# Kernel optimization log

Measured on AMD Instinct MI355X. Metric: run time of the kernel, lower is better.

Reference implementation:

```python
import jax, jax.numpy as jnp
import numpy as np

B, S, D, H, F = 4, 2048, 512, 8, 2048
HD = D // H
SCALE = HD ** -0.5


def layernorm(x, g, b, eps=1e-5):
    mu = jnp.mean(x, axis=-1, keepdims=True)
    var = jnp.var(x, axis=-1, keepdims=True)
    return (x - mu) * jax.lax.rsqrt(var + eps) * g + b


def setup_inputs() -> dict:
    key = jax.random.key(0)
    ks = jax.random.split(key, 10)
    s = 0.02
    return {
        "x": jax.random.normal(ks[0], (B, S, D), jnp.float32),
        "w_qkv": jax.random.normal(ks[1], (D, 3 * D), jnp.float32) * s,
        "b_qkv": jnp.zeros((3 * D,), jnp.float32),
        "w_o": jax.random.normal(ks[2], (D, D), jnp.float32) * s,
        "b_o": jnp.zeros((D,), jnp.float32),
        "w1": jax.random.normal(ks[3], (D, F), jnp.float32) * s,
        "b1": jnp.zeros((F,), jnp.float32),
        "w2": jax.random.normal(ks[4], (F, D), jnp.float32) * s,
        "b2": jnp.zeros((D,), jnp.float32),
        "g1": jnp.ones((D,), jnp.float32),
        "be1": jnp.zeros((D,), jnp.float32),
        "g2": jnp.ones((D,), jnp.float32),
        "be2": jnp.zeros((D,), jnp.float32),
    }


def reference(x, w_qkv, b_qkv, w_o, b_o, w1, b1, w2, b2, g1, be1, g2, be2):
    res = x
    qkv = x @ w_qkv + b_qkv                       # [B,S,3D]
    q, k, v = jnp.split(qkv, 3, axis=-1)          # each [B,S,D]
    # head partition: [B,S,D] -> [B,H,S,hd]
    def split_heads(t):
        return t.reshape(B, S, H, HD).transpose(0, 2, 1, 3)
    q, k, v = map(split_heads, (q, k, v))
    scores = jnp.einsum('bhqc,bhkc->bhqk', q, k) * SCALE
    weights = jax.nn.softmax(scores, axis=-1)
    out = jnp.einsum('bhqk,bhkc->bhqc', weights, v)
    out = out.transpose(0, 2, 1, 3).reshape(B, S, D)  # merge heads
    out = out @ w_o + b_o
    out = layernorm(out + res, g1, be1)
    res = out
    out = jax.nn.gelu(out @ w1 + b1, approximate=False) @ w2 + b2
    out = layernorm(out + res, g2, be2)
    return out
```

## Files before the change

kernel.cpp:

```cpp
#include <hip/hip_runtime.h>
#include <math.h>

constexpr int B = 4, S = 2048, D = 512, H = 8, HD = 64, F = 2048;
constexpr int M = B * S;
constexpr float C_QK = 0.125f * 1.44269504088896340736f;

typedef __bf16 bf16x8 __attribute__((ext_vector_type(8)));
typedef float  f32x4  __attribute__((ext_vector_type(4)));
typedef float  f32x16 __attribute__((ext_vector_type(16)));

static __device__ __forceinline__ short f2bf(float f) {
  return __builtin_bit_cast(short, (__bf16)f);
}

static __device__ __forceinline__ void gload16(const void* g, void* l) {
  __builtin_amdgcn_global_load_lds(
      (const __attribute__((address_space(1))) unsigned int*)g,
      (__attribute__((address_space(3))) unsigned int*)l, 16, 0, 0);
}

__global__ __launch_bounds__(256)
void prep_all(const float* __restrict__ x, short* __restrict__ xb,
              const float* __restrict__ w_qkv, short* __restrict__ wtq,
              const float* __restrict__ w_o,  short* __restrict__ wto,
              const float* __restrict__ w1,   short* __restrict__ wt1,
              const float* __restrict__ w2,   short* __restrict__ wt2) {
  __shared__ float tl[32][33];
  const int id = blockIdx.x;
  const int t = threadIdx.x;
  if (id < 4096) {
    int i = id * 256 + t;
    float4 v = ((const float4*)x)[i];
    ((short4*)xb)[i] = make_short4(f2bf(v.x), f2bf(v.y), f2bf(v.z), f2bf(v.w));
    return;
  }
  const float* in; short* out; int R, C, bx, by;
  if (id < 4864)      { int k = id - 4096; in = w_qkv; out = wtq; R = 512;  C = 1536; bx = k % 48; by = k / 48; }
  else if (id < 5120) { int k = id - 4864; in = w_o;   out = wto; R = 512;  C = 512;  bx = k % 16; by = k / 16; }
  else if (id < 6144) { int k = id - 5120; in = w1;    out = wt1; R = 512;  C = 2048; bx = k % 64; by = k / 64; }
  else                { int k = id - 6144; in = w2;    out = wt2; R = 2048; C = 512;  bx = k % 16; by = k / 16; }
  const int r0 = by * 32, c0 = bx * 32;
  const int tr = t >> 3, tc4 = (t & 7) * 4;
  float4 v = *(const float4*)&in[(size_t)(r0 + tr) * C + c0 + tc4];
  tl[tr][tc4] = v.x; tl[tr][tc4 + 1] = v.y; tl[tr][tc4 + 2] = v.z; tl[tr][tc4 + 3] = v.w;
  __syncthreads();
  short4 o = make_short4(f2bf(tl[tc4][tr]), f2bf(tl[tc4 + 1][tr]),
                         f2bf(tl[tc4 + 2][tr]), f2bf(tl[tc4 + 3][tr]));
  *(short4*)&out[(size_t)(c0 + tr) * R + r0 + tc4] = o;
}

template<int BM, int BN, int GELU, int EPI>
__global__ __launch_bounds__(256)
void gemm_bf16(const short* __restrict__ A, const short* __restrict__ Wt,
               const float* __restrict__ bias,
               float* __restrict__ Cf, short* __restrict__ Cb,
               short* __restrict__ qsw, short* __restrict__ ksw,
               short* __restrict__ vsw, int K, int N) {
  constexpr int MI = BM / 32, NI = BN / 32;
  __shared__ short As[2][BM * 64] __attribute__((aligned(16)));
  __shared__ short Bs[2][BN * 64] __attribute__((aligned(16)));
  const int t = threadIdx.x;
  const int w = t >> 6, l = t & 63, g = l >> 4, r = l & 15;
  const int wm = w >> 1, wn = w & 1;
  const int m0 = blockIdx.y * BM, n0 = blockIdx.x * BN;

  auto stage = [&](int buf, int k0) {
#pragma unroll
    for (int i = 0; i < BM / 32; ++i) {
      int q = i * 256 + t;
      int row = q >> 3, sl = (q & 7) ^ (row & 7);
      gload16(A + (size_t)(m0 + row) * K + k0 + sl * 8, (char*)As[buf] + q * 16);
    }
#pragma unroll
    for (int i = 0; i < BN / 32; ++i) {
      int q = i * 256 + t;
      int row = q >> 3, sl = (q & 7) ^ (row & 7);
      gload16(Wt + (size_t)(n0 + row) * K + k0 + sl * 8, (char*)Bs[buf] + q * 16);
    }
  };

  f32x4 acc[MI][NI] = {};
  const int NS = K >> 6;
  stage(0, 0);
  __syncthreads();
  for (int st = 0; st < NS; ++st) {
    const int cur = st & 1;
    if (st + 1 < NS) stage(cur ^ 1, (st + 1) << 6);
    const short* Ac = As[cur];
    const short* Bc = Bs[cur];
#pragma unroll
    for (int kh = 0; kh < 2; ++kh) {
      const int cc = kh * 4 + g;
      bf16x8 aF[MI], bF[NI];
#pragma unroll
      for (int mi = 0; mi < MI; ++mi) {
        const int row = wm * (MI * 16) + mi * 16 + r;
        aF[mi] = *(const bf16x8*)(Ac + row * 64 + ((cc ^ (r & 7)) << 3));
      }
#pragma unroll
      for (int ni = 0; ni < NI; ++ni) {
        const int row = wn * (NI * 16) + ni * 16 + r;
        bF[ni] = *(const bf16x8*)(Bc + row * 64 + ((cc ^ (r & 7)) << 3));
      }
#pragma unroll
      for (int mi = 0; mi < MI; ++mi)
#pragma unroll
        for (int ni = 0; ni < NI; ++ni)
          acc[mi][ni] = __builtin_amdgcn_mfma_f32_16x16x32_bf16(aF[mi], bF[ni], acc[mi][ni], 0, 0, 0);
    }
    __syncthreads();
  }

#pragma unroll
  for (int mi = 0; mi < MI; ++mi) {
#pragma unroll
    for (int ni = 0; ni < NI; ++ni) {
      const int n  = n0 + wn * (NI * 16) + ni * 16 + r;
      const int mB = m0 + wm * (MI * 16) + mi * 16 + g * 4;
      float vals[4];
#pragma unroll
      for (int j = 0; j < 4; ++j) {
        float v = acc[mi][ni][j] + bias[n];
        if (GELU) v = 0.5f * v * (1.0f + erff(v * 0.70710678118654752f));
        vals[j] = v;
      }
      if (EPI == 0) {
#pragma unroll
        for (int j = 0; j < 4; ++j) Cf[(size_t)(mB + j) * N + n] = vals[j];
      } else if (EPI == 1) {
#pragma unroll
        for (int j = 0; j < 4; ++j) Cb[(size_t)(mB + j) * N + n] = f2bf(vals[j]);
      } else {
        const int b = mB >> 11, s = mB & 2047;
        if (n < 512) {
          const int hh = n >> 6, d = n & 63;
          const size_t rb = (size_t)(b * 8 + hh) * 2048;
#pragma unroll
          for (int j = 0; j < 4; ++j)
            qsw[(rb + s + j) * 64 + (d ^ (((s + j) & 7) << 3))] = f2bf(vals[j] * C_QK);
        } else if (n < 1024) {
          const int hh = (n - 512) >> 6, d = (n - 512) & 63;
          const size_t rb = (size_t)(b * 8 + hh) * 2048;
#pragma unroll
          for (int j = 0; j < 4; ++j)
            ksw[(rb + s + j) * 64 + (d ^ (((s + j) & 7) << 3))] = f2bf(vals[j]);
        } else {
          const int hh = (n - 1024) >> 6, d = (n - 1024) & 63;
          short4 pk = make_short4(f2bf(vals[0]), f2bf(vals[1]), f2bf(vals[2]), f2bf(vals[3]));
          *(short4*)&vsw[(size_t)((b * 8 + hh) * 64 + d) * 2048 + (s ^ ((d & 7) << 3))] = pk;
        }
      }
    }
  }
}

__global__ __launch_bounds__(256, 4)
void attn_mfma(const short* __restrict__ qsw, const short* __restrict__ ksw,
               const short* __restrict__ vsw, short* __restrict__ Opart,
               float* __restrict__ Lpart) {
  __shared__ short Ks[64 * 64] __attribute__((aligned(16)));
  __shared__ short Vs[64 * 64] __attribute__((aligned(16)));
  const int t = threadIdx.x;
  const int w = t >> 6, l = t & 63;
  const int c = l & 31, hi = l >> 5;
  const int bh = blockIdx.y;
  const int q0 = blockIdx.x * 128;
  const int kbase = blockIdx.z * 1024;
  const short* qb = qsw + ((size_t)bh * 2048 + q0) * 64;
  const short* kb = ksw + (size_t)bh * 2048 * 64;
  const short* vb = vsw + (size_t)bh * 64 * 2048;

  const int qrow = w * 32 + c;
  const int swz = (c & 7) << 3;
  bf16x8 qf[4];
#pragma unroll
  for (int dc = 0; dc < 4; ++dc)
    qf[dc] = *(const bf16x8*)(qb + qrow * 64 + ((dc * 16 + hi * 8) ^ swz));

  f32x16 o0 = {}, o1 = {};
  float m_run = -3e38f, l_run = 0.0f;

  for (int ti = 0; ti < 16; ++ti) {
    const int kt = kbase + ti * 64;
    __syncthreads();
#pragma unroll
    for (int i = 0; i < 2; ++i) {
      int q = i * 256 + t;
      gload16(kb + (size_t)(kt + (q >> 3)) * 64 + (q & 7) * 8, (char*)Ks + q * 16);
    }
#pragma unroll
    for (int i = 0; i < 2; ++i) {
      int q = i * 256 + t;
      gload16(vb + (size_t)(q >> 3) * 2048 + kt + (q & 7) * 8, (char*)Vs + q * 16);
    }
    __syncthreads();

#pragma unroll
    for (int h2 = 0; h2 < 2; ++h2) {
      f32x16 s = {};
      __builtin_amdgcn_s_setprio(1);
#pragma unroll
      for (int dc = 0; dc < 4; ++dc) {
        const int koff = (dc * 16 + hi * 8) ^ swz;
        bf16x8 kf = *(const bf16x8*)(Ks + (h2 * 32 + c) * 64 + koff);
        s = __builtin_amdgcn_mfma_f32_32x32x16_bf16(kf, qf[dc], s, 0, 0, 0);
      }
      __builtin_amdgcn_s_setprio(0);

      float tmax = -3e38f;
#pragma unroll
      for (int j = 0; j < 16; ++j) tmax = fmaxf(tmax, s[j]);
      tmax = fmaxf(tmax, __shfl_xor(tmax, 32, 64));
      if (__any(tmax - m_run > 8.0f)) {
        float mnew = fmaxf(m_run, tmax);
        float rs = __builtin_amdgcn_exp2f(m_run - mnew);
        m_run = mnew;
        l_run *= rs;
#pragma unroll
        for (int j = 0; j < 16; ++j) {
          float rj = __shfl(rs, (j & 3) + 8 * (j >> 2) + 4 * hi, 64);
          o0[j] *= rj; o1[j] *= rj;
        }
      }
      float rsum = 0.0f;
#pragma unroll
      for (int j = 0; j < 16; ++j) {
        s[j] = __builtin_amdgcn_exp2f(s[j] - m_run);
        rsum += s[j];
      }
      rsum += __shfl_xor(rsum, 32, 64);
      l_run += rsum;

      __builtin_amdgcn_s_setprio(1);
#pragma unroll
      for (int kc = 0; kc < 2; ++kc) {
        const int jb = kc * 8;
        int u0, u1, v0, v1;
        asm("v_cvt_pk_bf16_f32 %0, %1, %2" : "=v"(u0) : "v"(s[jb + 0]), "v"(s[jb + 1]));
        asm("v_cvt_pk_bf16_f32 %0, %1, %2" : "=v"(u1) : "v"(s[jb + 2]), "v"(s[jb + 3]));
        asm("v_cvt_pk_bf16_f32 %0, %1, %2" : "=v"(v0) : "v"(s[jb + 4]), "v"(s[jb + 5]));
        asm("v_cvt_pk_bf16_f32 %0, %1, %2" : "=v"(v1) : "v"(s[jb + 6]), "v"(s[jb + 7]));
        asm volatile("v_permlane32_swap_b32 %0, %1" : "+v"(u0), "+v"(v0));
        asm volatile("v_permlane32_swap_b32 %0, %1" : "+v"(u1), "+v"(v1));
        int pw[4] = {u0, u1, v0, v1};
        bf16x8 pa = __builtin_bit_cast(bf16x8, *(int4*)pw);
        const int voff = ((h2 * 32 + kc * 16 + hi * 8)) ^ swz;
        bf16x8 vf0 = *(const bf16x8*)(Vs + c * 64 + voff);
        bf16x8 vf1 = *(const bf16x8*)(Vs + (32 + c) * 64 + voff);
        o0 = __builtin_amdgcn_mfma_f32_32x32x16_bf16(pa, vf0, o0, 0, 0, 0);
        o1 = __builtin_amdgcn_mfma_f32_32x32x16_bf16(pa, vf1, o1, 0, 0, 0);
      }
      __builtin_amdgcn_s_setprio(0);
    }
  }

  const size_t hrow = (size_t)blockIdx.z * (32 * 2048) + (size_t)bh * 2048;
  float inv = 1.0f / l_run;
  if (hi == 0)
    Lpart[hrow + q0 + w * 32 + c] = m_run + __builtin_log2f(l_run);
#pragma unroll
  for (int j = 0; j < 16; ++j) {
    const int q_rel = (j & 3) + 8 * (j >> 2) + 4 * hi;
    float invq = __shfl(inv, q_rel, 64);
    const size_t row = (hrow + q0 + w * 32 + q_rel) * 64;
    Opart[row + c]      = f2bf(o0[j] * invq);
    Opart[row + 32 + c] = f2bf(o1[j] * invq);
  }
}

__global__ __launch_bounds__(256)
void attn_combine(const short* __restrict__ Opart, const float* __restrict__ Lpart,
                  short* __restrict__ a_o) {
  const int idx = blockIdx.x * 256 + threadIdx.x;
  const int row = idx >> 3;
  const int d8 = (idx & 7) * 8;
  const float L0 = Lpart[row], L1 = Lpart[65536 + row];
  const float mx = fmaxf(L0, L1);
  const float w0 = __builtin_amdgcn_exp2f(L0 - mx), w1 = __builtin_amdgcn_exp2f(L1 - mx);
  const float inv = 1.0f / (w0 + w1);
  bf16x8 a = *(const bf16x8*)(Opart + (size_t)row * 64 + d8);
  bf16x8 b = *(const bf16x8*)(Opart + ((size_t)65536 + row) * 64 + d8);
  bf16x8 res;
#pragma unroll
  for (int i = 0; i < 8; ++i)
    res[i] = (__bf16)((w0 * (float)a[i] + w1 * (float)b[i]) * inv);
  const int bh = row >> 11, s = row & 2047;
  const int bb = bh >> 3, hh = bh & 7;
  *(bf16x8*)(a_o + ((size_t)(bb * 2048 + s)) * 512 + hh * 64 + d8) = res;
}

template<int WB>
__global__ __launch_bounds__(256)
void add_ln(const float* __restrict__ a, const float* __restrict__ res,
            const float* __restrict__ g_, const float* __restrict__ be,
            float* __restrict__ out, short* __restrict__ outb) {
  const int row = blockIdx.x;
  const int t = threadIdx.x;
  const size_t off = (size_t)row * D;
  float x0 = a[off + t] + res[off + t];
  float x1 = a[off + t + 256] + res[off + t + 256];
  float sum = x0 + x1;
  float sq  = x0 * x0 + x1 * x1;
#pragma unroll
  for (int o2 = 32; o2 > 0; o2 >>= 1) {
    sum += __shfl_down(sum, o2);
    sq  += __shfl_down(sq, o2);
  }
  __shared__ float ssum[4], ssq[4];
  const int wid = t >> 6;
  if ((t & 63) == 0) { ssum[wid] = sum; ssq[wid] = sq; }
  __syncthreads();
  if (t == 0) {
    ssum[0] = ssum[0] + ssum[1] + ssum[2] + ssum[3];
    ssq[0]  = ssq[0] + ssq[1] + ssq[2] + ssq[3];
  }
  __syncthreads();
  float mu   = ssum[0] * (1.0f / D);
  float var  = ssq[0] * (1.0f / D) - mu * mu;
  float rstd = rsqrtf(var + 1e-5f);
  float y0 = (x0 - mu) * rstd * g_[t] + be[t];
  float y1 = (x1 - mu) * rstd * g_[t + 256] + be[t + 256];
  out[off + t] = y0;
  out[off + t + 256] = y1;
  if (WB) {
    outb[off + t] = f2bf(y0);
    outb[off + t + 256] = f2bf(y1);
  }
}

extern "C" void kernel_launch(void* const* d_in, const int* in_sizes, int n_in,
                              void* d_out, int out_size, void* d_ws, size_t ws_size,
                              hipStream_t stream) {
  const float* x     = (const float*)d_in[0];
  const float* w_qkv = (const float*)d_in[1];
  const float* b_qkv = (const float*)d_in[2];
  const float* w_o   = (const float*)d_in[3];
  const float* b_o   = (const float*)d_in[4];
  const float* w1    = (const float*)d_in[5];
  const float* b1    = (const float*)d_in[6];
  const float* w2    = (const float*)d_in[7];
  const float* b2    = (const float*)d_in[8];
  const float* g1    = (const float*)d_in[9];
  const float* be1   = (const float*)d_in[10];
  const float* g2    = (const float*)d_in[11];
  const float* be2   = (const float*)d_in[12];
  float* out = (float*)d_out;
  (void)in_sizes; (void)n_in; (void)out_size; (void)ws_size;

  const size_t MD = (size_t)M * 512;
  short* q_sw = (short*)d_ws;
  short* k_sw = q_sw + MD;
  short* v_sw = k_sw + MD;
  short* a_o  = v_sw + MD;
  short* h    = q_sw;
  short* xb   = a_o + MD;
  short* ln1b = xb;
  short* wtq  = xb + MD;
  short* wto  = wtq + (size_t)1536 * 512;
  short* wt1  = wto + (size_t)512 * 512;
  short* wt2  = wt1 + (size_t)512 * 2048;
  float* buf  = (float*)(wt2 + (size_t)2048 * 512);
  float* ln1  = buf + MD;
  short* Opart = (short*)(ln1 + MD);
  float* Lpart = (float*)(Opart + (size_t)2 * 32 * 2048 * 64);

  prep_all<<<7168, 256, 0, stream>>>(x, xb, w_qkv, wtq, w_o, wto, w1, wt1, w2, wt2);

  gemm_bf16<128, 64, 0, 2><<<dim3(24, 64), 256, 0, stream>>>(
      xb, wtq, b_qkv, nullptr, nullptr, q_sw, k_sw, v_sw, 512, 1536);
  attn_mfma<<<dim3(16, 32, 2), 256, 0, stream>>>(q_sw, k_sw, v_sw, Opart, Lpart);
  attn_combine<<<2048, 256, 0, stream>>>(Opart, Lpart, a_o);
  gemm_bf16<64, 64, 0, 0><<<dim3(8, 128), 256, 0, stream>>>(
      a_o, wto, b_o, buf, nullptr, nullptr, nullptr, nullptr, 512, 512);
  add_ln<1><<<M, 256, 0, stream>>>(buf, x, g1, be1, ln1, ln1b);
  gemm_bf16<128, 64, 1, 1><<<dim3(32, 64), 256, 0, stream>>>(
      ln1b, wt1, b1, nullptr, h, nullptr, nullptr, nullptr, 512, 2048);
  gemm_bf16<64, 64, 0, 0><<<dim3(8, 128), 256, 0, stream>>>(
      h, wt2, b2, buf, nullptr, nullptr, nullptr, nullptr, 2048, 512);
  add_ln<0><<<M, 256, 0, stream>>>(buf, ln1, g2, be2, out, nullptr);
}
```

Before: 285.1 us.

## Use 128x128 GEMM tiles with split-K, and split attention KV four ways

The GEMM changes to fixed 128x128 tiles with a K-step of 32. It drops the double-buffered, swizzled LDS staging in favour of a single unswizzled buffer. Split-K=2 is added for the two N=512 GEMMs, and the partial sums are added inside add_ln, which now reads two inputs. Attention now splits the KV range into 4 chunks instead of 2, and the combine kernel merges 4 partials. Opart reuses buf as scratch. The larger tiles aim to improve operand reuse and the extra splits aim to raise parallelism. The costs are lost load/compute overlap, possible LDS bank conflicts, and more partial-result traffic.

New measurement: 291.2 us. 2.2% more time.

```diff
diff --git a/kernel.cpp b/kernel.cpp
--- a/kernel.cpp
+++ b/kernel.cpp
@@ -49,84 +49,70 @@
   *(short4*)&out[(size_t)(c0 + tr) * R + r0 + tc4] = o;
 }
 
-template<int BM, int BN, int GELU, int EPI>
+template<int SPLITK, int GELU, int EPI>
 __global__ __launch_bounds__(256)
 void gemm_bf16(const short* __restrict__ A, const short* __restrict__ Wt,
                const float* __restrict__ bias,
                float* __restrict__ Cf, short* __restrict__ Cb,
                short* __restrict__ qsw, short* __restrict__ ksw,
-               short* __restrict__ vsw, int K, int N) {
-  constexpr int MI = BM / 32, NI = BN / 32;
-  __shared__ short As[2][BM * 64] __attribute__((aligned(16)));
-  __shared__ short Bs[2][BN * 64] __attribute__((aligned(16)));
+               short* __restrict__ vsw, int K, int N, size_t pz) {
+  __shared__ short As[128 * 32] __attribute__((aligned(16)));
+  __shared__ short Bs[128 * 32] __attribute__((aligned(16)));
   const int t = threadIdx.x;
   const int w = t >> 6, l = t & 63, g = l >> 4, r = l & 15;
   const int wm = w >> 1, wn = w & 1;
-  const int m0 = blockIdx.y * BM, n0 = blockIdx.x * BN;
-
-  auto stage = [&](int buf, int k0) {
-#pragma unroll
-    for (int i = 0; i < BM / 32; ++i) {
+  const int m0 = blockIdx.y * 128, n0 = blockIdx.x * 128;
+  const int Kc = K / SPLITK;
+  const int kstart = blockIdx.z * Kc;
+
+  f32x4 acc[4][4] = {};
+  const int NS = Kc >> 5;
+  for (int st = 0; st < NS; ++st) {
+    const int k0 = kstart + (st << 5);
+    __syncthreads();
+#pragma unroll
+    for (int i = 0; i < 2; ++i) {
       int q = i * 256 + t;
-      int row = q >> 3, sl = (q & 7) ^ (row & 7);
-      gload16(A + (size_t)(m0 + row) * K + k0 + sl * 8, (char*)As[buf] + q * 16);
-    }
-#pragma unroll
-    for (int i = 0; i < BN / 32; ++i) {
+      gload16(A + (size_t)(m0 + (q >> 2)) * K + k0 + (q & 3) * 8, (char*)As + q * 16);
+    }
+#pragma unroll
+    for (int i = 0; i < 2; ++i) {
       int q = i * 256 + t;
-      int row = q >> 3, sl = (q & 7) ^ (row & 7);
-      gload16(Wt + (size_t)(n0 + row) * K + k0 + sl * 8, (char*)Bs[buf] + q * 16);
-    }
-  };
-
-  f32x4 acc[MI][NI] = {};
-  const int NS = K >> 6;
-  stage(0, 0);
-  __syncthreads();
-  for (int st = 0; st < NS; ++st) {
-    const int cur = st & 1;
-    if (st + 1 < NS) stage(cur ^ 1, (st + 1) << 6);
-    const short* Ac = As[cur];
-    const short* Bc = Bs[cur];
-#pragma unroll
-    for (int kh = 0; kh < 2; ++kh) {
-      const int cc = kh * 4 + g;
-      bf16x8 aF[MI], bF[NI];
-#pragma unroll
-      for (int mi = 0; mi < MI; ++mi) {
-        const int row = wm * (MI * 16) + mi * 16 + r;
-        aF[mi] = *(const bf16x8*)(Ac + row * 64 + ((cc ^ (r & 7)) << 3));
-      }
-#pragma unroll
-      for (int ni = 0; ni < NI; ++ni) {
-        const int row = wn * (NI * 16) + ni * 16 + r;
-        bF[ni] = *(const bf16x8*)(Bc + row * 64 + ((cc ^ (r & 7)) << 3));
-      }
-#pragma unroll
-      for (int mi = 0; mi < MI; ++mi)
-#pragma unroll
-        for (int ni = 0; ni < NI; ++ni)
-          acc[mi][ni] = __builtin_amdgcn_mfma_f32_16x16x32_bf16(aF[mi], bF[ni], acc[mi][ni], 0, 0, 0);
+      gload16(Wt + (size_t)(n0 + (q >> 2)) * K + k0 + (q & 3) * 8, (char*)Bs + q * 16);
     }
     __syncthreads();
-  }
-
-#pragma unroll
-  for (int mi = 0; mi < MI; ++mi) {
-#pragma unroll
-    for (int ni = 0; ni < NI; ++ni) {
-      const int n  = n0 + wn * (NI * 16) + ni * 16 + r;
-      const int mB = m0 + wm * (MI * 16) + mi * 16 + g * 4;
+    bf16x8 aF[4], bF[4];
+#pragma unroll
+    for (int mi = 0; mi < 4; ++mi)
+      aF[mi] = *(const bf16x8*)(As + (wm * 64 + mi * 16 + r) * 32 + g * 8);
+#pragma unroll
+    for (int ni = 0; ni < 4; ++ni)
+      bF[ni] = *(const bf16x8*)(Bs + (wn * 64 + ni * 16 + r) * 32 + g * 8);
+#pragma unroll
+    for (int mi = 0; mi < 4; ++mi)
+#pragma unroll
+      for (int ni = 0; ni < 4; ++ni)
+        acc[mi][ni] = __builtin_amdgcn_mfma_f32_16x16x32_bf16(aF[mi], bF[ni], acc[mi][ni], 0, 0, 0);
+  }
+
+  float* Cfz = Cf + (size_t)blockIdx.z * pz;
+  const float bscale = (SPLITK > 1 && blockIdx.z != 0) ? 0.0f : 1.0f;
+#pragma unroll
+  for (int mi = 0; mi < 4; ++mi) {
+#pragma unroll
+    for (int ni = 0; ni < 4; ++ni) {
+      const int n  = n0 + wn * 64 + ni * 16 + r;
+      const int mB = m0 + wm * 64 + mi * 16 + g * 4;
       float vals[4];
 #pragma unroll
       for (int j = 0; j < 4; ++j) {
-        float v = acc[mi][ni][j] + bias[n];
+        float v = acc[mi][ni][j] + bias[n] * bscale;
         if (GELU) v = 0.5f * v * (1.0f + erff(v * 0.70710678118654752f));
         vals[j] = v;
       }
       if (EPI == 0) {
 #pragma unroll
-        for (int j = 0; j < 4; ++j) Cf[(size_t)(mB + j) * N + n] = vals[j];
+        for (int j = 0; j < 4; ++j) Cfz[(size_t)(mB + j) * N + n] = vals[j];
       } else if (EPI == 1) {
 #pragma unroll
         for (int j = 0; j < 4; ++j) Cb[(size_t)(mB + j) * N + n] = f2bf(vals[j]);
@@ -165,7 +151,7 @@
   const int c = l & 31, hi = l >> 5;
   const int bh = blockIdx.y;
   const int q0 = blockIdx.x * 128;
-  const int kbase = blockIdx.z * 1024;
+  const int kbase = blockIdx.z * 512;
   const short* qb = qsw + ((size_t)bh * 2048 + q0) * 64;
   const short* kb = ksw + (size_t)bh * 2048 * 64;
   const short* vb = vsw + (size_t)bh * 64 * 2048;
@@ -180,7 +166,7 @@
   f32x16 o0 = {}, o1 = {};
   float m_run = -3e38f, l_run = 0.0f;
 
-  for (int ti = 0; ti < 16; ++ti) {
+  for (int ti = 0; ti < 8; ++ti) {
     const int kt = kbase + ti * 64;
     __syncthreads();
 #pragma unroll
@@ -274,24 +260,33 @@
   const int idx = blockIdx.x * 256 + threadIdx.x;
   const int row = idx >> 3;
   const int d8 = (idx & 7) * 8;
-  const float L0 = Lpart[row], L1 = Lpart[65536 + row];
-  const float mx = fmaxf(L0, L1);
-  const float w0 = __builtin_amdgcn_exp2f(L0 - mx), w1 = __builtin_amdgcn_exp2f(L1 - mx);
-  const float inv = 1.0f / (w0 + w1);
-  bf16x8 a = *(const bf16x8*)(Opart + (size_t)row * 64 + d8);
-  bf16x8 b = *(const bf16x8*)(Opart + ((size_t)65536 + row) * 64 + d8);
+  float L[4];
+#pragma unroll
+  for (int z = 0; z < 4; ++z) L[z] = Lpart[z * 65536 + row];
+  float mx = fmaxf(fmaxf(L[0], L[1]), fmaxf(L[2], L[3]));
+  float wz[4], wsum = 0.0f;
+#pragma unroll
+  for (int z = 0; z < 4; ++z) { wz[z] = __builtin_amdgcn_exp2f(L[z] - mx); wsum += wz[z]; }
+  const float inv = 1.0f / wsum;
+  float acc[8] = {};
+#pragma unroll
+  for (int z = 0; z < 4; ++z) {
+    bf16x8 a = *(const bf16x8*)(Opart + ((size_t)z * 65536 + row) * 64 + d8);
+#pragma unroll
+    for (int i = 0; i < 8; ++i) acc[i] += wz[z] * (float)a[i];
+  }
   bf16x8 res;
 #pragma unroll
-  for (int i = 0; i < 8; ++i)
-    res[i] = (__bf16)((w0 * (float)a[i] + w1 * (float)b[i]) * inv);
+  for (int i = 0; i < 8; ++i) res[i] = (__bf16)(acc[i] * inv);
   const int bh = row >> 11, s = row & 2047;
   const int bb = bh >> 3, hh = bh & 7;
   *(bf16x8*)(a_o + ((size_t)(bb * 2048 + s)) * 512 + hh * 64 + d8) = res;
 }
 
-template<int WB>
+template<int WB, int TWO>
 __global__ __launch_bounds__(256)
-void add_ln(const float* __restrict__ a, const float* __restrict__ res,
+void add_ln(const float* __restrict__ a, const float* __restrict__ a2,
+            const float* __restrict__ res,
             const float* __restrict__ g_, const float* __restrict__ be,
             float* __restrict__ out, short* __restrict__ outb) {
   const int row = blockIdx.x;
@@ -299,6 +294,7 @@
   const size_t off = (size_t)row * D;
   float x0 = a[off + t] + res[off + t];
   float x1 = a[off + t + 256] + res[off + t + 256];
+  if (TWO) { x0 += a2[off + t]; x1 += a2[off + t + 256]; }
   float sum = x0 + x1;
   float sq  = x0 * x0 + x1 * x1;
 #pragma unroll
@@ -361,21 +357,22 @@
   short* wt2  = wt1 + (size_t)512 * 2048;
   float* buf  = (float*)(wt2 + (size_t)2048 * 512);
   float* ln1  = buf + MD;
-  short* Opart = (short*)(ln1 + MD);
-  float* Lpart = (float*)(Opart + (size_t)2 * 32 * 2048 * 64);
+  float* buf2 = ln1 + MD;
+  float* Lpart = buf2 + MD;
+  short* Opart = (short*)buf;
 
   prep_all<<<7168, 256, 0, stream>>>(x, xb, w_qkv, wtq, w_o, wto, w1, wt1, w2, wt2);
 
-  gemm_bf16<128, 64, 0, 2><<<dim3(24, 64), 256, 0, stream>>>(
-      xb, wtq, b_qkv, nullptr, nullptr, q_sw, k_sw, v_sw, 512, 1536);
-  attn_mfma<<<dim3(16, 32, 2), 256, 0, stream>>>(q_sw, k_sw, v_sw, Opart, Lpart);
+  gemm_bf16<1, 0, 2><<<dim3(12, 64), 256, 0, stream>>>(
+      xb, wtq, b_qkv, nullptr, nullptr, q_sw, k_sw, v_sw, 512, 1536, 0);
+  attn_mfma<<<dim3(16, 32, 4), 256, 0, stream>>>(q_sw, k_sw, v_sw, Opart, Lpart);
   attn_combine<<<2048, 256, 0, stream>>>(Opart, Lpart, a_o);
-  gemm_bf16<64, 64, 0, 0><<<dim3(8, 128), 256, 0, stream>>>(
-      a_o, wto, b_o, buf, nullptr, nullptr, nullptr, nullptr, 512, 512);
-  add_ln<1><<<M, 256, 0, stream>>>(buf, x, g1, be1, ln1, ln1b);
-  gemm_bf16<128, 64, 1, 1><<<dim3(32, 64), 256, 0, stream>>>(
-      ln1b, wt1, b1, nullptr, h, nullptr, nullptr, nullptr, 512, 2048);
-  gemm_bf16<64, 64, 0, 0><<<dim3(8, 128), 256, 0, stream>>>(
-      h, wt2, b2, buf, nullptr, nullptr, nullptr, nullptr, 2048, 512);
-  add_ln<0><<<M, 256, 0, stream>>>(buf, ln1, g2, be2, out, nullptr);
-}
+  gemm_bf16<2, 0, 0><<<dim3(4, 64, 2), 256, 0, stream>>>(
+      a_o, wto, b_o, buf, nullptr, nullptr, nullptr, nullptr, 512, 512, (size_t)2 * MD);
+  add_ln<1, 1><<<M, 256, 0, stream>>>(buf, buf2, x, g1, be1, ln1, ln1b);
+  gemm_bf16<1, 1, 1><<<dim3(16, 64), 256, 0, stream>>>(
+      ln1b, wt1, b1, nullptr, h, nullptr, nullptr, nullptr, 512, 2048, 0);
+  gemm_bf16<2, 0, 0><<<dim3(4, 64, 2), 256, 0, stream>>>(
+      h, wt2, b2, buf, nullptr, nullptr, nullptr, nullptr, 2048, 512, (size_t)2 * MD);
+  add_ln<0, 1><<<M, 256, 0, stream>>>(buf, buf2, ln1, g2, be2, out, nullptr);
+}
```
